# Kernel optimization log

Hardware: AMD Instinct MI355X
Metric: run time of the kernel (lower is better)

The kernel has to match this reference:

```python
import jax, jax.numpy as jnp
import numpy as np

TOKENS, D_MODEL, D_FF, RANK = 16384, 1024, 2816, 16


def setup_inputs() -> dict:
    key = jax.random.key(0)
    ks = jax.random.split(key, 7)
    s = lambda k, shp, scale: jax.random.normal(k, shp, dtype=jnp.float32) * scale
    return {
        "x": s(ks[0], (TOKENS, D_MODEL), 1.0),
        "W_gate_up": s(ks[1], (D_MODEL, 2 * D_FF), 0.02),
        "A_gate_up": s(ks[2], (D_MODEL, RANK), 0.02),
        "B_gate_up": s(ks[3], (RANK, 2 * D_FF), 0.02),
        "W_down": s(ks[4], (D_FF, D_MODEL), 0.02),
        "A_down": s(ks[5], (D_FF, RANK), 0.02),
        "B_down": s(ks[6], (RANK, D_MODEL), 0.02),
    }


def reference(x, W_gate_up, A_gate_up, B_gate_up, W_down, A_down, B_down):
    # gate_up_proj: base GEMM + LoRA low-rank correction
    gate_up = x @ W_gate_up + (x @ A_gate_up) @ B_gate_up  # [T, 2*D_FF]
    gate, up = jnp.split(gate_up, 2, axis=-1)
    h = jax.nn.silu(gate) * up  # SiluAndMul, [T, D_FF]
    # down_proj: base GEMM + LoRA correction
    out = h @ W_down + (h @ A_down) @ B_down  # [T, D_MODEL]
    return out
```

## Files before the change

kernel.cpp:

```cpp
#include <hip/hip_runtime.h>


typedef __bf16 bf16_t;
typedef __bf16 bf16x4 __attribute__((ext_vector_type(4)));
typedef __bf16 bf16x8 __attribute__((ext_vector_type(8)));
typedef float f32x4 __attribute__((ext_vector_type(4)));

#define TOKENS 16384
#define DMODEL 1024
#define DFF    2816
#define N2F    5632

#define BARM() asm volatile("s_barrier" ::: "memory")
#define VMW(n) asm volatile("s_waitcnt vmcnt(" #n ")" ::: "memory")
#define MFMA(d, va, vb) d = __builtin_amdgcn_mfma_f32_16x16x32_bf16(va, vb, d, 0, 0, 0)
#define LD8(p) (*(const bf16x8*)(p))
#define SGB(m, n) __builtin_amdgcn_sched_group_barrier(m, n, 0)
#define SGB_INTERLEAVE() do {                                                     \
    SGB(0x010, 4);                                                                \
    SGB(0x100, 2); SGB(0x008, 5);                                                 \
    SGB(0x100, 2); SGB(0x008, 5);                                                 \
    SGB(0x100, 2); SGB(0x008, 5);                                                 \
    SGB(0x100, 2); SGB(0x008, 5);                                                 \
    SGB(0x100, 2); SGB(0x008, 5);                                                 \
    SGB(0x100, 2); SGB(0x008, 7); } while (0)

__device__ __forceinline__ void gload16(const bf16_t* g, bf16_t* l) {
    __builtin_amdgcn_global_load_lds(
        (const __attribute__((address_space(1))) void*)g,
        (__attribute__((address_space(3))) void*)l, 16, 0, 0);
}

template<int KTOT, int NTOT>
__global__ __launch_bounds__(256) void prep_weff(
        const float* __restrict__ W, const float* __restrict__ A,
        const float* __restrict__ B, bf16_t* __restrict__ Wt) {
    __shared__ float Ws[64][65];
    __shared__ float As[64][17];
    __shared__ float Bs[16][64];
    const int t = threadIdx.x;
    const int k0 = blockIdx.x * 64, n0 = blockIdx.y * 64;
    #pragma unroll
    for (int i = 0; i < 16; ++i) {
        int row = i * 4 + t / 64, col = t % 64;
        Ws[row][col] = W[(size_t)(k0 + row) * NTOT + n0 + col];
    }
    #pragma unroll
    for (int i = 0; i < 4; ++i) {
        int idx = i * 256 + t;
        As[idx / 16][idx % 16] = A[(size_t)(k0 + idx / 16) * 16 + idx % 16];
    }
    #pragma unroll
    for (int i = 0; i < 4; ++i) {
        int idx = i * 256 + t;
        Bs[idx / 64][idx % 64] = B[(size_t)(idx / 64) * NTOT + n0 + idx % 64];
    }
    __syncthreads();
    const int kl = t % 64;
    #pragma unroll
    for (int j = 0; j < 16; ++j) {
        int nl = j * 4 + t / 64;
        float val = Ws[kl][nl];
        #pragma unroll
        for (int r = 0; r < 16; ++r) val += As[kl][r] * Bs[r][nl];
        Wt[(size_t)(n0 + nl) * KTOT + k0 + kl] = (bf16_t)val;
    }
}

__global__ __launch_bounds__(256) void conv_bf16(
        const float* __restrict__ in, bf16_t* __restrict__ out, int n4) {
    int i = blockIdx.x * 256 + threadIdx.x;
    if (i < n4) {
        float4 v = ((const float4*)in)[i];
        bf16x4 o;
        o.x = (bf16_t)v.x; o.y = (bf16_t)v.y; o.z = (bf16_t)v.z; o.w = (bf16_t)v.w;
        ((bf16x4*)out)[i] = o;
    }
}

__global__ __launch_bounds__(512, 2) void gemm1(
        const bf16_t* __restrict__ X, const bf16_t* __restrict__ Wt,
        bf16_t* __restrict__ H) {
    __shared__ bf16_t lds[65536];
    const int t = threadIdx.x, l = t & 63;
    const int wid = t >> 6, wr = wid >> 2, wc = wid & 3;
    const int l15 = l & 15, lhi = l >> 4;
    const int wgl = ((int)blockIdx.x & 7) * 176 + ((int)blockIdx.x >> 3);
    const int tf = wgl % 22, tm = wgl / 22;
    const int mbase = tm * 256, fbase = tf * 128;
    const int srow = t >> 2;
    const int sc8 = ((t & 3) ^ (srow & 3)) * 8;
    const bf16_t* gA  = X + (size_t)(mbase + srow) * DMODEL + sc8;
    const bf16_t* gA2 = gA + (size_t)128 * DMODEL;
    const bf16_t* gBg = Wt + (size_t)(fbase + srow) * DMODEL + sc8;
    const bf16_t* gBu = Wt + (size_t)(DFF + fbase + srow) * DMODEL + sc8;
    const int rsw = (lhi ^ (l15 & 3)) * 8;
    const int aoff = (wr * 128 + l15) * 32 + rsw;
    const int boff = 8192 + (wc * 32 + l15) * 32 + rsw;

    f32x4 accg[8][2] = {}, accu[8][2] = {};
    bf16x8 a0[8], g0[2], u0[2], a1[8], g1[2], u1[2];
    const int NT1 = DMODEL / 32;

#define G1_STAGE(kt) do { const int kc = (kt) * 32;                               \
    bf16_t* p = lds + (((kt) & 3) << 14) + wid * 512;                             \
    gload16(gA  + kc, p);                                                         \
    gload16(gA2 + kc, p + 4096);                                                  \
    gload16(gBg + kc, p + 8192);                                                  \
    gload16(gBu + kc, p + 12288); } while (0)
#define G1_READ(aa, gg, uu, bi) do {                                              \
    const bf16_t* _pa = lds + ((bi) << 14) + aoff;                                \
    aa[0] = LD8(_pa);        aa[1] = LD8(_pa + 512);                              \
    aa[2] = LD8(_pa + 1024); aa[3] = LD8(_pa + 1536);                             \
    aa[4] = LD8(_pa + 2048); aa[5] = LD8(_pa + 2560);                             \
    aa[6] = LD8(_pa + 3072); aa[7] = LD8(_pa + 3584);                             \
    const bf16_t* _pb = lds + ((bi) << 14) + boff;                                \
    gg[0] = LD8(_pb);        gg[1] = LD8(_pb + 512);                              \
    uu[0] = LD8(_pb + 4096); uu[1] = LD8(_pb + 4608); } while (0)
#define G1_MFMA(aa, gg, uu) do {                                                  \
    _Pragma("unroll")                                                             \
    for (int m = 0; m < 8; ++m) {                                                 \
        MFMA(accg[m][0], aa[m], gg[0]); MFMA(accu[m][0], aa[m], uu[0]);           \
        MFMA(accg[m][1], aa[m], gg[1]); MFMA(accu[m][1], aa[m], uu[1]);           \
    } } while (0)
#define G1_ITER(kt, aaU, ggU, uuU, aaR, ggR, uuR) do {                            \
    VMW(4); BARM();                                                               \
    if ((kt) + 3 < NT1) G1_STAGE((kt) + 3);                                       \
    G1_READ(aaR, ggR, uuR, ((kt) + 1) & 3);                                       \
    G1_MFMA(aaU, ggU, uuU);                                                       \
    SGB_INTERLEAVE(); } while (0)

    G1_STAGE(0); G1_STAGE(1); G1_STAGE(2);
    VMW(8); BARM();
    G1_READ(a0, g0, u0, 0);
    for (int kt2 = 0; kt2 < NT1 - 2; kt2 += 2) {
        G1_ITER(kt2,     a0, g0, u0, a1, g1, u1);
        G1_ITER(kt2 + 1, a1, g1, u1, a0, g0, u0);
    }
    VMW(0); BARM();
    G1_READ(a1, g1, u1, (NT1 - 1) & 3);
    G1_MFMA(a0, g0, u0);
    G1_MFMA(a1, g1, u1);
#undef G1_ITER
#undef G1_STAGE
#undef G1_READ
#undef G1_MFMA

    #pragma unroll
    for (int m = 0; m < 8; ++m)
        #pragma unroll
        for (int n = 0; n < 2; ++n)
            #pragma unroll
            for (int r = 0; r < 4; ++r) {
                int row = mbase + wr * 128 + m * 16 + lhi * 4 + r;
                int col = fbase + wc * 32 + n * 16 + l15;
                float g = accg[m][n][r], u = accu[m][n][r];
                H[(size_t)row * DFF + col] = (bf16_t)(g / (1.0f + __expf(-g)) * u);
            }
}

__global__ __launch_bounds__(512, 2) void gemm2(
        const bf16_t* __restrict__ Hm, const bf16_t* __restrict__ Wt,
        float* __restrict__ O) {
    __shared__ bf16_t lds[65536];
    const int t = threadIdx.x, l = t & 63;
    const int wid = t >> 6, wr = wid >> 2, wc = wid & 3;
    const int l15 = l & 15, lhi = l >> 4;
    const int wgl = ((int)blockIdx.x & 7) * 32 + ((int)blockIdx.x >> 3);
    const int tn = wgl % 4, tm = wgl / 4;
    const int mbase = tm * 256, nbase = tn * 256;
    const int srow = t >> 2;
    const int sc8 = ((t & 3) ^ (srow & 3)) * 8;
    const bf16_t* gA  = Hm + (size_t)(mbase + srow) * DFF + sc8;
    const bf16_t* gA2 = gA + (size_t)128 * DFF;
    const bf16_t* gB  = Wt + (size_t)(nbase + srow) * DFF + sc8;
    const bf16_t* gB2 = gB + (size_t)128 * DFF;
    const int rsw = (lhi ^ (l15 & 3)) * 8;
    const int aoff = (wr * 128 + l15) * 32 + rsw;
    const int boff = 8192 + (wc * 64 + l15) * 32 + rsw;

    f32x4 acc[8][4] = {};
    bf16x8 a0[8], b0[4], a1[8], b1[4];
    const int NT2 = DFF / 32;

#define G2_STAGE(kt) do { const int kc = (kt) * 32;                               \
    bf16_t* p = lds + (((kt) & 3) << 14) + wid * 512;                             \
    gload16(gA  + kc, p);                                                         \
    gload16(gA2 + kc, p + 4096);                                                  \
    gload16(gB  + kc, p + 8192);                                                  \
    gload16(gB2 + kc, p + 12288); } while (0)
#define G2_READ(aa, bb, bi) do {                                                  \
    const bf16_t* _pa = lds + ((bi) << 14) + aoff;                                \
    aa[0] = LD8(_pa);        aa[1] = LD8(_pa + 512);                              \
    aa[2] = LD8(_pa + 1024); aa[3] = LD8(_pa + 1536);                             \
    aa[4] = LD8(_pa + 2048); aa[5] = LD8(_pa + 2560);                             \
    aa[6] = LD8(_pa + 3072); aa[7] = LD8(_pa + 3584);                             \
    const bf16_t* _pb = lds + ((bi) << 14) + boff;                                \
    bb[0] = LD8(_pb);        bb[1] = LD8(_pb + 512);                              \
    bb[2] = LD8(_pb + 1024); bb[3] = LD8(_pb + 1536); } while (0)
#define G2_MFMA(aa, bb) do {                                                      \
    _Pragma("unroll")                                                             \
    for (int m = 0; m < 8; ++m) {                                                 \
        MFMA(acc[m][0], aa[m], bb[0]); MFMA(acc[m][1], aa[m], bb[1]);             \
        MFMA(acc[m][2], aa[m], bb[2]); MFMA(acc[m][3], aa[m], bb[3]);             \
    } } while (0)
#define G2_ITER(kt, aaU, bbU, aaR, bbR) do {                                      \
    VMW(4); BARM();                                                               \
    if ((kt) + 3 < NT2) G2_STAGE((kt) + 3);                                       \
    G2_READ(aaR, bbR, ((kt) + 1) & 3);                                            \
    G2_MFMA(aaU, bbU);                                                            \
    SGB_INTERLEAVE(); } while (0)

    G2_STAGE(0); G2_STAGE(1); G2_STAGE(2);
    VMW(8); BARM();
    G2_READ(a0, b0, 0);
    for (int kt2 = 0; kt2 < NT2 - 2; kt2 += 2) {
        G2_ITER(kt2,     a0, b0, a1, b1);
        G2_ITER(kt2 + 1, a1, b1, a0, b0);
    }
    VMW(0); BARM();
    G2_READ(a1, b1, (NT2 - 1) & 3);
    G2_MFMA(a0, b0);
    G2_MFMA(a1, b1);
#undef G2_STAGE
#undef G2_READ
#undef G2_MFMA
#undef G2_ITER

    #pragma unroll
    for (int m = 0; m < 8; ++m)
        #pragma unroll
        for (int n = 0; n < 4; ++n)
            #pragma unroll
            for (int r = 0; r < 4; ++r) {
                int row = mbase + wr * 128 + m * 16 + lhi * 4 + r;
                int col = nbase + wc * 64 + n * 16 + l15;
                O[(size_t)row * DMODEL + col] = acc[m][n][r];
            }
}

extern "C" void kernel_launch(void* const* d_in, const int* in_sizes, int n_in,
                              void* d_out, int out_size, void* d_ws, size_t ws_size,
                              hipStream_t stream) {
    const float* x   = (const float*)d_in[0];
    const float* Wgu = (const float*)d_in[1];
    const float* Agu = (const float*)d_in[2];
    const float* Bgu = (const float*)d_in[3];
    const float* Wd  = (const float*)d_in[4];
    const float* Ad  = (const float*)d_in[5];
    const float* Bd  = (const float*)d_in[6];
    float* out = (float*)d_out;
    char* ws = (char*)d_ws;

    bf16_t* wgut = (bf16_t*)(ws);
    bf16_t* wdt  = (bf16_t*)(ws + 11534336);
    bf16_t* xb   = (bf16_t*)(ws + 17301504);
    bf16_t* hb   = (bf16_t*)(ws + 50855936);

    prep_weff<DMODEL, N2F><<<dim3(DMODEL / 64, N2F / 64), 256, 0, stream>>>(
        Wgu, Agu, Bgu, wgut);
    prep_weff<DFF, DMODEL><<<dim3(DFF / 64, DMODEL / 64), 256, 0, stream>>>(
        Wd, Ad, Bd, wdt);
    conv_bf16<<<(TOKENS * DMODEL / 4) / 256, 256, 0, stream>>>(
        x, xb, TOKENS * DMODEL / 4);
    gemm1<<<22 * 64, 512, 0, stream>>>(xb, wgut, hb);
    gemm2<<<8 * 32, 512, 0, stream>>>(hb, wdt, out);
}
```

Before: 327.9 us.

## Load A operand directly from global into registers, stage only B in LDS

Both GEMM kernels now read the A tile (X or H) straight from global memory into registers with one tile of lookahead, and stage only the weight (B) tiles through LDS. This halves LDS allocation and removes the LDS write/read round trip for A. The MFMA/load interleave schedule is also changed to match. In exchange, the four waves sharing a row block each fetch the same A data from global or L2 separately, and A load latency is hidden by only one iteration.

```diff
diff --git a/kernel.cpp b/kernel.cpp
--- a/kernel.cpp
+++ b/kernel.cpp
@@ -16,14 +16,10 @@
 #define MFMA(d, va, vb) d = __builtin_amdgcn_mfma_f32_16x16x32_bf16(va, vb, d, 0, 0, 0)
 #define LD8(p) (*(const bf16x8*)(p))
 #define SGB(m, n) __builtin_amdgcn_sched_group_barrier(m, n, 0)
-#define SGB_INTERLEAVE() do {                                                     \
-    SGB(0x010, 4);                                                                \
-    SGB(0x100, 2); SGB(0x008, 5);                                                 \
-    SGB(0x100, 2); SGB(0x008, 5);                                                 \
-    SGB(0x100, 2); SGB(0x008, 5);                                                 \
-    SGB(0x100, 2); SGB(0x008, 5);                                                 \
-    SGB(0x100, 2); SGB(0x008, 5);                                                 \
-    SGB(0x100, 2); SGB(0x008, 7); } while (0)
+#define SGB_PATTERN() do {                                                        \
+    SGB(0x010, 4); SGB(0x100, 4); SGB(0x008, 4);                                  \
+    SGB(0x010, 4); SGB(0x008, 4);                                                 \
+    SGB(0x010, 2); SGB(0x008, 24); } while (0)
 
 __device__ __forceinline__ void gload16(const bf16_t* g, bf16_t* l) {
     __builtin_amdgcn_global_load_lds(
@@ -81,7 +77,7 @@
 __global__ __launch_bounds__(512, 2) void gemm1(
         const bf16_t* __restrict__ X, const bf16_t* __restrict__ Wt,
         bf16_t* __restrict__ H) {
-    __shared__ bf16_t lds[65536];
+    __shared__ bf16_t lds[32768];
     const int t = threadIdx.x, l = t & 63;
     const int wid = t >> 6, wr = wid >> 2, wc = wid & 3;
     const int l15 = l & 15, lhi = l >> 4;
@@ -90,33 +86,30 @@
     const int mbase = tm * 256, fbase = tf * 128;
     const int srow = t >> 2;
     const int sc8 = ((t & 3) ^ (srow & 3)) * 8;
-    const bf16_t* gA  = X + (size_t)(mbase + srow) * DMODEL + sc8;
-    const bf16_t* gA2 = gA + (size_t)128 * DMODEL;
+    const bf16_t* gA0 = X + (size_t)(mbase + wr * 128 + l15) * DMODEL + lhi * 8;
     const bf16_t* gBg = Wt + (size_t)(fbase + srow) * DMODEL + sc8;
     const bf16_t* gBu = Wt + (size_t)(DFF + fbase + srow) * DMODEL + sc8;
     const int rsw = (lhi ^ (l15 & 3)) * 8;
-    const int aoff = (wr * 128 + l15) * 32 + rsw;
-    const int boff = 8192 + (wc * 32 + l15) * 32 + rsw;
+    const int bgoff = (wc * 32 + l15) * 32 + rsw;
+    const int buoff = bgoff + 4096;
 
     f32x4 accg[8][2] = {}, accu[8][2] = {};
     bf16x8 a0[8], g0[2], u0[2], a1[8], g1[2], u1[2];
     const int NT1 = DMODEL / 32;
 
-#define G1_STAGE(kt) do { const int kc = (kt) * 32;                               \
-    bf16_t* p = lds + (((kt) & 3) << 14) + wid * 512;                             \
-    gload16(gA  + kc, p);                                                         \
-    gload16(gA2 + kc, p + 4096);                                                  \
-    gload16(gBg + kc, p + 8192);                                                  \
-    gload16(gBu + kc, p + 12288); } while (0)
-#define G1_READ(aa, gg, uu, bi) do {                                              \
-    const bf16_t* _pa = lds + ((bi) << 14) + aoff;                                \
-    aa[0] = LD8(_pa);        aa[1] = LD8(_pa + 512);                              \
-    aa[2] = LD8(_pa + 1024); aa[3] = LD8(_pa + 1536);                             \
-    aa[4] = LD8(_pa + 2048); aa[5] = LD8(_pa + 2560);                             \
-    aa[6] = LD8(_pa + 3072); aa[7] = LD8(_pa + 3584);                             \
-    const bf16_t* _pb = lds + ((bi) << 14) + boff;                                \
-    gg[0] = LD8(_pb);        gg[1] = LD8(_pb + 512);                              \
-    uu[0] = LD8(_pb + 4096); uu[1] = LD8(_pb + 4608); } while (0)
+#define G1_ALOAD(aa, kt) do { const bf16_t* _p = gA0 + (kt) * 32;                 \
+    aa[0] = LD8(_p);                 aa[1] = LD8(_p + 16 * DMODEL);               \
+    aa[2] = LD8(_p + 32 * DMODEL);   aa[3] = LD8(_p + 48 * DMODEL);               \
+    aa[4] = LD8(_p + 64 * DMODEL);   aa[5] = LD8(_p + 80 * DMODEL);               \
+    aa[6] = LD8(_p + 96 * DMODEL);   aa[7] = LD8(_p + 112 * DMODEL); } while (0)
+#define G1_BSTAGE(kt) do { const int kc = (kt) * 32;                              \
+    bf16_t* p = lds + (((kt) & 3) << 13) + wid * 512;                             \
+    gload16(gBg + kc, p);                                                         \
+    gload16(gBu + kc, p + 4096); } while (0)
+#define G1_BREAD(gg, uu, bi) do {                                                 \
+    const bf16_t* _b = lds + ((bi) << 13);                                        \
+    gg[0] = LD8(_b + bgoff);        gg[1] = LD8(_b + bgoff + 512);                \
+    uu[0] = LD8(_b + buoff);        uu[1] = LD8(_b + buoff + 512); } while (0)
 #define G1_MFMA(aa, gg, uu) do {                                                  \
     _Pragma("unroll")                                                             \
     for (int m = 0; m < 8; ++m) {                                                 \
@@ -124,26 +117,31 @@
         MFMA(accg[m][1], aa[m], gg[1]); MFMA(accu[m][1], aa[m], uu[1]);           \
     } } while (0)
 #define G1_ITER(kt, aaU, ggU, uuU, aaR, ggR, uuR) do {                            \
-    VMW(4); BARM();                                                               \
-    if ((kt) + 3 < NT1) G1_STAGE((kt) + 3);                                       \
-    G1_READ(aaR, ggR, uuR, ((kt) + 1) & 3);                                       \
+    VMW(2); BARM();                                                               \
+    G1_ALOAD(aaR, (kt) + 1);                                                      \
+    if ((kt) + 3 < NT1) G1_BSTAGE((kt) + 3);                                      \
+    G1_BREAD(ggR, uuR, ((kt) + 1) & 3);                                           \
     G1_MFMA(aaU, ggU, uuU);                                                       \
-    SGB_INTERLEAVE(); } while (0)
-
-    G1_STAGE(0); G1_STAGE(1); G1_STAGE(2);
-    VMW(8); BARM();
-    G1_READ(a0, g0, u0, 0);
+    SGB_PATTERN(); } while (0)
+
+    G1_BSTAGE(0); G1_BSTAGE(1); G1_BSTAGE(2);
+    G1_ALOAD(a0, 0);
+    VMW(0); BARM();
+    G1_BREAD(g0, u0, 0);
     for (int kt2 = 0; kt2 < NT1 - 2; kt2 += 2) {
         G1_ITER(kt2,     a0, g0, u0, a1, g1, u1);
         G1_ITER(kt2 + 1, a1, g1, u1, a0, g0, u0);
     }
     VMW(0); BARM();
-    G1_READ(a1, g1, u1, (NT1 - 1) & 3);
+    G1_ALOAD(a1, NT1 - 1);
+    G1_BREAD(g1, u1, (NT1 - 1) & 3);
     G1_MFMA(a0, g0, u0);
+    VMW(0);
     G1_MFMA(a1, g1, u1);
 #undef G1_ITER
-#undef G1_STAGE
-#undef G1_READ
+#undef G1_ALOAD
+#undef G1_BSTAGE
+#undef G1_BREAD
 #undef G1_MFMA
 
     #pragma unroll
@@ -162,7 +160,7 @@
 __global__ __launch_bounds__(512, 2) void gemm2(
         const bf16_t* __restrict__ Hm, const bf16_t* __restrict__ Wt,
         float* __restrict__ O) {
-    __shared__ bf16_t lds[65536];
+    __shared__ bf16_t lds[32768];
     const int t = threadIdx.x, l = t & 63;
     const int wid = t >> 6, wr = wid >> 2, wc = wid & 3;
     const int l15 = l & 15, lhi = l >> 4;
@@ -171,33 +169,29 @@
     const int mbase = tm * 256, nbase = tn * 256;
     const int srow = t >> 2;
     const int sc8 = ((t & 3) ^ (srow & 3)) * 8;
-    const bf16_t* gA  = Hm + (size_t)(mbase + srow) * DFF + sc8;
-    const bf16_t* gA2 = gA + (size_t)128 * DFF;
+    const bf16_t* gA0 = Hm + (size_t)(mbase + wr * 128 + l15) * DFF + lhi * 8;
     const bf16_t* gB  = Wt + (size_t)(nbase + srow) * DFF + sc8;
     const bf16_t* gB2 = gB + (size_t)128 * DFF;
     const int rsw = (lhi ^ (l15 & 3)) * 8;
-    const int aoff = (wr * 128 + l15) * 32 + rsw;
-    const int boff = 8192 + (wc * 64 + l15) * 32 + rsw;
+    const int boff = (wc * 64 + l15) * 32 + rsw;
 
     f32x4 acc[8][4] = {};
     bf16x8 a0[8], b0[4], a1[8], b1[4];
     const int NT2 = DFF / 32;
 
-#define G2_STAGE(kt) do { const int kc = (kt) * 32;                               \
-    bf16_t* p = lds + (((kt) & 3) << 14) + wid * 512;                             \
-    gload16(gA  + kc, p);                                                         \
-    gload16(gA2 + kc, p + 4096);                                                  \
-    gload16(gB  + kc, p + 8192);                                                  \
-    gload16(gB2 + kc, p + 12288); } while (0)
-#define G2_READ(aa, bb, bi) do {                                                  \
-    const bf16_t* _pa = lds + ((bi) << 14) + aoff;                                \
-    aa[0] = LD8(_pa);        aa[1] = LD8(_pa + 512);                              \
-    aa[2] = LD8(_pa + 1024); aa[3] = LD8(_pa + 1536);                             \
-    aa[4] = LD8(_pa + 2048); aa[5] = LD8(_pa + 2560);                             \
-    aa[6] = LD8(_pa + 3072); aa[7] = LD8(_pa + 3584);                             \
-    const bf16_t* _pb = lds + ((bi) << 14) + boff;                                \
-    bb[0] = LD8(_pb);        bb[1] = LD8(_pb + 512);                              \
-    bb[2] = LD8(_pb + 1024); bb[3] = LD8(_pb + 1536); } while (0)
+#define G2_ALOAD(aa, kt) do { const bf16_t* _p = gA0 + (kt) * 32;                 \
+    aa[0] = LD8(_p);               aa[1] = LD8(_p + 16 * DFF);                    \
+    aa[2] = LD8(_p + 32 * DFF);    aa[3] = LD8(_p + 48 * DFF);                    \
+    aa[4] = LD8(_p + 64 * DFF);    aa[5] = LD8(_p + 80 * DFF);                    \
+    aa[6] = LD8(_p + 96 * DFF);    aa[7] = LD8(_p + 112 * DFF); } while (0)
+#define G2_BSTAGE(kt) do { const int kc = (kt) * 32;                              \
+    bf16_t* p = lds + (((kt) & 3) << 13) + wid * 512;                             \
+    gload16(gB  + kc, p);                                                         \
+    gload16(gB2 + kc, p + 4096); } while (0)
+#define G2_BREAD(bb, bi) do {                                                     \
+    const bf16_t* _b = lds + ((bi) << 13) + boff;                                 \
+    bb[0] = LD8(_b);        bb[1] = LD8(_b + 512);                                \
+    bb[2] = LD8(_b + 1024); bb[3] = LD8(_b + 1536); } while (0)
 #define G2_MFMA(aa, bb) do {                                                      \
     _Pragma("unroll")                                                             \
     for (int m = 0; m < 8; ++m) {                                                 \
@@ -205,27 +199,32 @@
         MFMA(acc[m][2], aa[m], bb[2]); MFMA(acc[m][3], aa[m], bb[3]);             \
     } } while (0)
 #define G2_ITER(kt, aaU, bbU, aaR, bbR) do {                                      \
-    VMW(4); BARM();                                                               \
-    if ((kt) + 3 < NT2) G2_STAGE((kt) + 3);                                       \
-    G2_READ(aaR, bbR, ((kt) + 1) & 3);                                            \
+    VMW(2); BARM();                                                               \
+    G2_ALOAD(aaR, (kt) + 1);                                                      \
+    if ((kt) + 3 < NT2) G2_BSTAGE((kt) + 3);                                      \
+    G2_BREAD(bbR, ((kt) + 1) & 3);                                                \
     G2_MFMA(aaU, bbU);                                                            \
-    SGB_INTERLEAVE(); } while (0)
-
-    G2_STAGE(0); G2_STAGE(1); G2_STAGE(2);
-    VMW(8); BARM();
-    G2_READ(a0, b0, 0);
+    SGB_PATTERN(); } while (0)
+
+    G2_BSTAGE(0); G2_BSTAGE(1); G2_BSTAGE(2);
+    G2_ALOAD(a0, 0);
+    VMW(0); BARM();
+    G2_BREAD(b0, 0);
     for (int kt2 = 0; kt2 < NT2 - 2; kt2 += 2) {
         G2_ITER(kt2,     a0, b0, a1, b1);
         G2_ITER(kt2 + 1, a1, b1, a0, b0);
     }
     VMW(0); BARM();
-    G2_READ(a1, b1, (NT2 - 1) & 3);
+    G2_ALOAD(a1, NT2 - 1);
+    G2_BREAD(b1, (NT2 - 1) & 3);
     G2_MFMA(a0, b0);
+    VMW(0);
     G2_MFMA(a1, b1);
-#undef G2_STAGE
-#undef G2_READ
+#undef G2_ITER
+#undef G2_ALOAD
+#undef G2_BSTAGE
+#undef G2_BREAD
 #undef G2_MFMA
-#undef G2_ITER
 
     #pragma unroll
     for (int m = 0; m < 8; ++m)
```

After: 693.2 us. +111.4%, slower.

## Shrink GEMM workgroups to 4 waves with 3-stage LDS ring buffer

Applied to the files above, without the earlier changes.

Both GEMMs move from 512-thread workgroups to 256-thread ones, which halves the N-tile (gemm1 64 FF columns, gemm2 128 output columns) and doubles the grid. The LDS pipeline changes from a 4-deep buffer with vmcnt(4) waits to a 3-deep ring with full vmcnt(0) waits, and LDS use drops to 72KB. The intent is more workgroups per CU and smaller LDS for better occupancy, plus a better load balance for gemm2, which previously had only 256 blocks. In exchange each block reuses the A tile across fewer columns, so global traffic for A goes up. The full wait also gives the loads less time to overlap with compute, and the scheduling-group pattern is retuned to match.

```diff
diff --git a/kernel.cpp b/kernel.cpp
--- a/kernel.cpp
+++ b/kernel.cpp
@@ -16,14 +16,14 @@
 #define MFMA(d, va, vb) d = __builtin_amdgcn_mfma_f32_16x16x32_bf16(va, vb, d, 0, 0, 0)
 #define LD8(p) (*(const bf16x8*)(p))
 #define SGB(m, n) __builtin_amdgcn_sched_group_barrier(m, n, 0)
-#define SGB_INTERLEAVE() do {                                                     \
-    SGB(0x010, 4);                                                                \
-    SGB(0x100, 2); SGB(0x008, 5);                                                 \
-    SGB(0x100, 2); SGB(0x008, 5);                                                 \
-    SGB(0x100, 2); SGB(0x008, 5);                                                 \
-    SGB(0x100, 2); SGB(0x008, 5);                                                 \
-    SGB(0x100, 2); SGB(0x008, 5);                                                 \
-    SGB(0x100, 2); SGB(0x008, 7); } while (0)
+#define SGB_PATTERN() do {                                                        \
+    SGB(0x010, 6);                                                                \
+    SGB(0x100, 2); SGB(0x008, 5);                                                 \
+    SGB(0x100, 2); SGB(0x008, 5);                                                 \
+    SGB(0x100, 2); SGB(0x008, 5);                                                 \
+    SGB(0x100, 2); SGB(0x008, 5);                                                 \
+    SGB(0x100, 2); SGB(0x008, 6);                                                 \
+    SGB(0x100, 2); SGB(0x008, 6); } while (0)
 
 __device__ __forceinline__ void gload16(const bf16_t* g, bf16_t* l) {
     __builtin_amdgcn_global_load_lds(
@@ -78,45 +78,46 @@
     }
 }
 
-__global__ __launch_bounds__(512, 2) void gemm1(
+__global__ __launch_bounds__(256, 2) void gemm1(
         const bf16_t* __restrict__ X, const bf16_t* __restrict__ Wt,
         bf16_t* __restrict__ H) {
-    __shared__ bf16_t lds[65536];
+    __shared__ bf16_t lds[36864];
     const int t = threadIdx.x, l = t & 63;
-    const int wid = t >> 6, wr = wid >> 2, wc = wid & 3;
+    const int wid = t >> 6, wr = wid >> 1, wc = wid & 1;
     const int l15 = l & 15, lhi = l >> 4;
-    const int wgl = ((int)blockIdx.x & 7) * 176 + ((int)blockIdx.x >> 3);
-    const int tf = wgl % 22, tm = wgl / 22;
-    const int mbase = tm * 256, fbase = tf * 128;
+    const int wgl = ((int)blockIdx.x & 7) * 352 + ((int)blockIdx.x >> 3);
+    const int tf = wgl % 44, tm = wgl / 44;
+    const int mbase = tm * 256, fbase = tf * 64;
     const int srow = t >> 2;
     const int sc8 = ((t & 3) ^ (srow & 3)) * 8;
     const bf16_t* gA  = X + (size_t)(mbase + srow) * DMODEL + sc8;
-    const bf16_t* gA2 = gA + (size_t)128 * DMODEL;
     const bf16_t* gBg = Wt + (size_t)(fbase + srow) * DMODEL + sc8;
     const bf16_t* gBu = Wt + (size_t)(DFF + fbase + srow) * DMODEL + sc8;
     const int rsw = (lhi ^ (l15 & 3)) * 8;
     const int aoff = (wr * 128 + l15) * 32 + rsw;
-    const int boff = 8192 + (wc * 32 + l15) * 32 + rsw;
+    const int bgoff = 8192 + (wc * 32 + l15) * 32 + rsw;
 
     f32x4 accg[8][2] = {}, accu[8][2] = {};
     bf16x8 a0[8], g0[2], u0[2], a1[8], g1[2], u1[2];
     const int NT1 = DMODEL / 32;
 
-#define G1_STAGE(kt) do { const int kc = (kt) * 32;                               \
-    bf16_t* p = lds + (((kt) & 3) << 14) + wid * 512;                             \
-    gload16(gA  + kc, p);                                                         \
-    gload16(gA2 + kc, p + 4096);                                                  \
+#define G1_STAGE(kt, bi) do { const int kc = (kt) * 32;                           \
+    bf16_t* p = lds + (bi) * 12288 + wid * 512;                                   \
+    gload16(gA + kc, p);                                                          \
+    gload16(gA + (size_t)64 * DMODEL + kc, p + 2048);                             \
+    gload16(gA + (size_t)128 * DMODEL + kc, p + 4096);                            \
+    gload16(gA + (size_t)192 * DMODEL + kc, p + 6144);                            \
     gload16(gBg + kc, p + 8192);                                                  \
-    gload16(gBu + kc, p + 12288); } while (0)
+    gload16(gBu + kc, p + 10240); } while (0)
 #define G1_READ(aa, gg, uu, bi) do {                                              \
-    const bf16_t* _pa = lds + ((bi) << 14) + aoff;                                \
+    const bf16_t* _pa = lds + (bi) * 12288 + aoff;                                \
     aa[0] = LD8(_pa);        aa[1] = LD8(_pa + 512);                              \
     aa[2] = LD8(_pa + 1024); aa[3] = LD8(_pa + 1536);                             \
     aa[4] = LD8(_pa + 2048); aa[5] = LD8(_pa + 2560);                             \
     aa[6] = LD8(_pa + 3072); aa[7] = LD8(_pa + 3584);                             \
-    const bf16_t* _pb = lds + ((bi) << 14) + boff;                                \
+    const bf16_t* _pb = lds + (bi) * 12288 + bgoff;                               \
     gg[0] = LD8(_pb);        gg[1] = LD8(_pb + 512);                              \
-    uu[0] = LD8(_pb + 4096); uu[1] = LD8(_pb + 4608); } while (0)
+    uu[0] = LD8(_pb + 2048); uu[1] = LD8(_pb + 2560); } while (0)
 #define G1_MFMA(aa, gg, uu) do {                                                  \
     _Pragma("unroll")                                                             \
     for (int m = 0; m < 8; ++m) {                                                 \
@@ -124,21 +125,24 @@
         MFMA(accg[m][1], aa[m], gg[1]); MFMA(accu[m][1], aa[m], uu[1]);           \
     } } while (0)
 #define G1_ITER(kt, aaU, ggU, uuU, aaR, ggR, uuR) do {                            \
-    VMW(4); BARM();                                                               \
-    if ((kt) + 3 < NT1) G1_STAGE((kt) + 3);                                       \
-    G1_READ(aaR, ggR, uuR, ((kt) + 1) & 3);                                       \
+    VMW(0); BARM();                                                               \
+    if ((kt) + 2 < NT1) G1_STAGE((kt) + 2, bS);                                   \
+    G1_READ(aaR, ggR, uuR, bR);                                                   \
     G1_MFMA(aaU, ggU, uuU);                                                       \
-    SGB_INTERLEAVE(); } while (0)
-
-    G1_STAGE(0); G1_STAGE(1); G1_STAGE(2);
-    VMW(8); BARM();
+    SGB_PATTERN();                                                                \
+    bR = (bR == 2) ? 0 : bR + 1;                                                  \
+    bS = (bS == 2) ? 0 : bS + 1; } while (0)
+
+    G1_STAGE(0, 0); G1_STAGE(1, 1);
+    VMW(0); BARM();
     G1_READ(a0, g0, u0, 0);
+    int bR = 1, bS = 2;
     for (int kt2 = 0; kt2 < NT1 - 2; kt2 += 2) {
         G1_ITER(kt2,     a0, g0, u0, a1, g1, u1);
         G1_ITER(kt2 + 1, a1, g1, u1, a0, g0, u0);
     }
     VMW(0); BARM();
-    G1_READ(a1, g1, u1, (NT1 - 1) & 3);
+    G1_READ(a1, g1, u1, (NT1 - 1) % 3);
     G1_MFMA(a0, g0, u0);
     G1_MFMA(a1, g1, u1);
 #undef G1_ITER
@@ -159,22 +163,20 @@
             }
 }
 
-__global__ __launch_bounds__(512, 2) void gemm2(
+__global__ __launch_bounds__(256, 2) void gemm2(
         const bf16_t* __restrict__ Hm, const bf16_t* __restrict__ Wt,
         float* __restrict__ O) {
-    __shared__ bf16_t lds[65536];
+    __shared__ bf16_t lds[36864];
     const int t = threadIdx.x, l = t & 63;
-    const int wid = t >> 6, wr = wid >> 2, wc = wid & 3;
+    const int wid = t >> 6, wr = wid >> 1, wc = wid & 1;
     const int l15 = l & 15, lhi = l >> 4;
-    const int wgl = ((int)blockIdx.x & 7) * 32 + ((int)blockIdx.x >> 3);
-    const int tn = wgl % 4, tm = wgl / 4;
-    const int mbase = tm * 256, nbase = tn * 256;
+    const int wgl = ((int)blockIdx.x & 7) * 64 + ((int)blockIdx.x >> 3);
+    const int tn = wgl % 8, tm = wgl / 8;
+    const int mbase = tm * 256, nbase = tn * 128;
     const int srow = t >> 2;
     const int sc8 = ((t & 3) ^ (srow & 3)) * 8;
-    const bf16_t* gA  = Hm + (size_t)(mbase + srow) * DFF + sc8;
-    const bf16_t* gA2 = gA + (size_t)128 * DFF;
-    const bf16_t* gB  = Wt + (size_t)(nbase + srow) * DFF + sc8;
-    const bf16_t* gB2 = gB + (size_t)128 * DFF;
+    const bf16_t* gA = Hm + (size_t)(mbase + srow) * DFF + sc8;
+    const bf16_t* gB = Wt + (size_t)(nbase + srow) * DFF + sc8;
     const int rsw = (lhi ^ (l15 & 3)) * 8;
     const int aoff = (wr * 128 + l15) * 32 + rsw;
     const int boff = 8192 + (wc * 64 + l15) * 32 + rsw;
@@ -183,19 +185,21 @@
     bf16x8 a0[8], b0[4], a1[8], b1[4];
     const int NT2 = DFF / 32;
 
-#define G2_STAGE(kt) do { const int kc = (kt) * 32;                               \
-    bf16_t* p = lds + (((kt) & 3) << 14) + wid * 512;                             \
-    gload16(gA  + kc, p);                                                         \
-    gload16(gA2 + kc, p + 4096);                                                  \
-    gload16(gB  + kc, p + 8192);                                                  \
-    gload16(gB2 + kc, p + 12288); } while (0)
+#define G2_STAGE(kt, bi) do { const int kc = (kt) * 32;                           \
+    bf16_t* p = lds + (bi) * 12288 + wid * 512;                                   \
+    gload16(gA + kc, p);                                                          \
+    gload16(gA + (size_t)64 * DFF + kc, p + 2048);                                \
+    gload16(gA + (size_t)128 * DFF + kc, p + 4096);                               \
+    gload16(gA + (size_t)192 * DFF + kc, p + 6144);                               \
+    gload16(gB + kc, p + 8192);                                                   \
+    gload16(gB + (size_t)64 * DFF + kc, p + 10240); } while (0)
 #define G2_READ(aa, bb, bi) do {                                                  \
-    const bf16_t* _pa = lds + ((bi) << 14) + aoff;                                \
+    const bf16_t* _pa = lds + (bi) * 12288 + aoff;                                \
     aa[0] = LD8(_pa);        aa[1] = LD8(_pa + 512);                              \
     aa[2] = LD8(_pa + 1024); aa[3] = LD8(_pa + 1536);                             \
     aa[4] = LD8(_pa + 2048); aa[5] = LD8(_pa + 2560);                             \
     aa[6] = LD8(_pa + 3072); aa[7] = LD8(_pa + 3584);                             \
-    const bf16_t* _pb = lds + ((bi) << 14) + boff;                                \
+    const bf16_t* _pb = lds + (bi) * 12288 + boff;                                \
     bb[0] = LD8(_pb);        bb[1] = LD8(_pb + 512);                              \
     bb[2] = LD8(_pb + 1024); bb[3] = LD8(_pb + 1536); } while (0)
 #define G2_MFMA(aa, bb) do {                                                      \
@@ -205,27 +209,30 @@
         MFMA(acc[m][2], aa[m], bb[2]); MFMA(acc[m][3], aa[m], bb[3]);             \
     } } while (0)
 #define G2_ITER(kt, aaU, bbU, aaR, bbR) do {                                      \
-    VMW(4); BARM();                                                               \
-    if ((kt) + 3 < NT2) G2_STAGE((kt) + 3);                                       \
-    G2_READ(aaR, bbR, ((kt) + 1) & 3);                                            \
+    VMW(0); BARM();                                                               \
+    if ((kt) + 2 < NT2) G2_STAGE((kt) + 2, bS);                                   \
+    G2_READ(aaR, bbR, bR);                                                        \
     G2_MFMA(aaU, bbU);                                                            \
-    SGB_INTERLEAVE(); } while (0)
-
-    G2_STAGE(0); G2_STAGE(1); G2_STAGE(2);
-    VMW(8); BARM();
+    SGB_PATTERN();                                                                \
+    bR = (bR == 2) ? 0 : bR + 1;                                                  \
+    bS = (bS == 2) ? 0 : bS + 1; } while (0)
+
+    G2_STAGE(0, 0); G2_STAGE(1, 1);
+    VMW(0); BARM();
     G2_READ(a0, b0, 0);
+    int bR = 1, bS = 2;
     for (int kt2 = 0; kt2 < NT2 - 2; kt2 += 2) {
         G2_ITER(kt2,     a0, b0, a1, b1);
         G2_ITER(kt2 + 1, a1, b1, a0, b0);
     }
     VMW(0); BARM();
-    G2_READ(a1, b1, (NT2 - 1) & 3);
+    G2_READ(a1, b1, (NT2 - 1) % 3);
     G2_MFMA(a0, b0);
     G2_MFMA(a1, b1);
+#undef G2_ITER
 #undef G2_STAGE
 #undef G2_READ
 #undef G2_MFMA
-#undef G2_ITER
 
     #pragma unroll
     for (int m = 0; m < 8; ++m)
@@ -263,6 +270,6 @@
         Wd, Ad, Bd, wdt);
     conv_bf16<<<(TOKENS * DMODEL / 4) / 256, 256, 0, stream>>>(
         x, xb, TOKENS * DMODEL / 4);
-    gemm1<<<22 * 64, 512, 0, stream>>>(xb, wgut, hb);
-    gemm2<<<8 * 32, 512, 0, stream>>>(hb, wdt, out);
-}
+    gemm1<<<44 * 64, 256, 0, stream>>>(xb, wgut, hb);
+    gemm2<<<8 * 64, 256, 0, stream>>>(hb, wdt, out);
+}
```

After: 337.0 us. 2.8% more time.

## Restructure GEMM main loops to two k-tiles per barrier with paired staging

Applied to the files above, without the earlier changes.

Both GEMM kernels now handle two k-tiles per iteration. Each iteration waits with vmcnt(0), passes one barrier, and issues global-to-LDS loads for the next pair of tiles. This replaces the previous one-tile-per-barrier loop that waited with vmcnt(4), and it halves the barrier count. The cost is a shallower effective prefetch distance, since the full drain each iteration may expose global load latency. The sched_group_barrier pattern is extended to cover the larger unrolled body.

```diff
diff --git a/kernel.cpp b/kernel.cpp
--- a/kernel.cpp
+++ b/kernel.cpp
@@ -16,13 +16,19 @@
 #define MFMA(d, va, vb) d = __builtin_amdgcn_mfma_f32_16x16x32_bf16(va, vb, d, 0, 0, 0)
 #define LD8(p) (*(const bf16x8*)(p))
 #define SGB(m, n) __builtin_amdgcn_sched_group_barrier(m, n, 0)
-#define SGB_INTERLEAVE() do {                                                     \
-    SGB(0x010, 4);                                                                \
-    SGB(0x100, 2); SGB(0x008, 5);                                                 \
-    SGB(0x100, 2); SGB(0x008, 5);                                                 \
-    SGB(0x100, 2); SGB(0x008, 5);                                                 \
-    SGB(0x100, 2); SGB(0x008, 5);                                                 \
-    SGB(0x100, 2); SGB(0x008, 5);                                                 \
+#define SGB_PATTERN2() do {                                                       \
+    SGB(0x010, 8);                                                                \
+    SGB(0x100, 2); SGB(0x008, 5);                                                 \
+    SGB(0x100, 2); SGB(0x008, 5);                                                 \
+    SGB(0x100, 2); SGB(0x008, 5);                                                 \
+    SGB(0x100, 2); SGB(0x008, 5);                                                 \
+    SGB(0x100, 2); SGB(0x008, 5);                                                 \
+    SGB(0x100, 2); SGB(0x008, 5);                                                 \
+    SGB(0x100, 2); SGB(0x008, 5);                                                 \
+    SGB(0x100, 2); SGB(0x008, 5);                                                 \
+    SGB(0x100, 2); SGB(0x008, 5);                                                 \
+    SGB(0x100, 2); SGB(0x008, 5);                                                 \
+    SGB(0x100, 2); SGB(0x008, 7);                                                 \
     SGB(0x100, 2); SGB(0x008, 7); } while (0)
 
 __device__ __forceinline__ void gload16(const bf16_t* g, bf16_t* l) {
@@ -123,25 +129,23 @@
         MFMA(accg[m][0], aa[m], gg[0]); MFMA(accu[m][0], aa[m], uu[0]);           \
         MFMA(accg[m][1], aa[m], gg[1]); MFMA(accu[m][1], aa[m], uu[1]);           \
     } } while (0)
-#define G1_ITER(kt, aaU, ggU, uuU, aaR, ggR, uuR) do {                            \
-    VMW(4); BARM();                                                               \
-    if ((kt) + 3 < NT1) G1_STAGE((kt) + 3);                                       \
-    G1_READ(aaR, ggR, uuR, ((kt) + 1) & 3);                                       \
-    G1_MFMA(aaU, ggU, uuU);                                                       \
-    SGB_INTERLEAVE(); } while (0)
-
-    G1_STAGE(0); G1_STAGE(1); G1_STAGE(2);
-    VMW(8); BARM();
+
+    G1_STAGE(0); G1_STAGE(1);
+    VMW(0); BARM();
+    G1_STAGE(2); G1_STAGE(3);
     G1_READ(a0, g0, u0, 0);
-    for (int kt2 = 0; kt2 < NT1 - 2; kt2 += 2) {
-        G1_ITER(kt2,     a0, g0, u0, a1, g1, u1);
-        G1_ITER(kt2 + 1, a1, g1, u1, a0, g0, u0);
-    }
-    VMW(0); BARM();
-    G1_READ(a1, g1, u1, (NT1 - 1) & 3);
+    G1_READ(a1, g1, u1, 1);
     G1_MFMA(a0, g0, u0);
+    for (int s2 = 2; s2 <= NT1 - 2; s2 += 2) {
+        VMW(0); BARM();
+        if (s2 + 2 < NT1) { G1_STAGE(s2 + 2); G1_STAGE(s2 + 3); }
+        G1_READ(a0, g0, u0, s2 & 3);
+        G1_MFMA(a1, g1, u1);
+        G1_READ(a1, g1, u1, (s2 + 1) & 3);
+        G1_MFMA(a0, g0, u0);
+        SGB_PATTERN2();
+    }
     G1_MFMA(a1, g1, u1);
-#undef G1_ITER
 #undef G1_STAGE
 #undef G1_READ
 #undef G1_MFMA
@@ -204,28 +208,26 @@
         MFMA(acc[m][0], aa[m], bb[0]); MFMA(acc[m][1], aa[m], bb[1]);             \
         MFMA(acc[m][2], aa[m], bb[2]); MFMA(acc[m][3], aa[m], bb[3]);             \
     } } while (0)
-#define G2_ITER(kt, aaU, bbU, aaR, bbR) do {                                      \
-    VMW(4); BARM();                                                               \
-    if ((kt) + 3 < NT2) G2_STAGE((kt) + 3);                                       \
-    G2_READ(aaR, bbR, ((kt) + 1) & 3);                                            \
-    G2_MFMA(aaU, bbU);                                                            \
-    SGB_INTERLEAVE(); } while (0)
-
-    G2_STAGE(0); G2_STAGE(1); G2_STAGE(2);
-    VMW(8); BARM();
+
+    G2_STAGE(0); G2_STAGE(1);
+    VMW(0); BARM();
+    G2_STAGE(2); G2_STAGE(3);
     G2_READ(a0, b0, 0);
-    for (int kt2 = 0; kt2 < NT2 - 2; kt2 += 2) {
-        G2_ITER(kt2,     a0, b0, a1, b1);
-        G2_ITER(kt2 + 1, a1, b1, a0, b0);
-    }
-    VMW(0); BARM();
-    G2_READ(a1, b1, (NT2 - 1) & 3);
+    G2_READ(a1, b1, 1);
     G2_MFMA(a0, b0);
+    for (int s2 = 2; s2 <= NT2 - 2; s2 += 2) {
+        VMW(0); BARM();
+        if (s2 + 2 < NT2) { G2_STAGE(s2 + 2); G2_STAGE(s2 + 3); }
+        G2_READ(a0, b0, s2 & 3);
+        G2_MFMA(a1, b1);
+        G2_READ(a1, b1, (s2 + 1) & 3);
+        G2_MFMA(a0, b0);
+        SGB_PATTERN2();
+    }
     G2_MFMA(a1, b1);
 #undef G2_STAGE
 #undef G2_READ
 #undef G2_MFMA
-#undef G2_ITER
 
     #pragma unroll
     for (int m = 0; m < 8; ++m)
```

Measured after the change: 327.6 us. Within noise of the previous version (-0.1%).
